# Performance work log

Hardware: AMD Instinct MI355X
Metric: run time of the kernel (lower is better)

Reference implementation:

```python
import jax, jax.numpy as jnp
import numpy as np
import math

B, S, DIM, H = 2, 2048, 1024, 16
DH = DIM // H          # 64, per-head dim
DFF = 2048             # FCLayer hidden
NEG = -1.0e9


def setup_inputs() -> dict:
    key = jax.random.key(0)
    ks = jax.random.split(key, 10)
    glorot = jax.nn.initializers.glorot_uniform()
    de_x = jax.random.normal(ks[0], (B, S, DIM), dtype=jnp.float32)
    en_x = jax.random.normal(ks[1], (B, S, DIM), dtype=jnp.float32)
    # causal mask: 1.0 where attention is disallowed (upper triangle)
    mask = jnp.triu(jnp.ones((S, S), dtype=jnp.float32), k=1)
    # Stacked per-head projection weights for the (shared) attn_heads.
    Wq = glorot(ks[2], (H, DIM, DH), jnp.float32)
    Wk = glorot(ks[3], (H, DIM, DH), jnp.float32)
    Wv = glorot(ks[4], (H, DIM, DH), jnp.float32)
    W1 = glorot(ks[5], (DIM, DFF), jnp.float32)
    b1 = jnp.zeros((DFF,), jnp.float32)
    W2 = glorot(ks[6], (DFF, DIM), jnp.float32)
    b2 = jnp.zeros((DIM,), jnp.float32)
    return {"de_x": de_x, "en_x": en_x, "mask": mask,
            "Wq": Wq, "Wk": Wk, "Wv": Wv,
            "W1": W1, "b1": b1, "W2": W2, "b2": b2}


def _multihead(q_x, k_x, v_x, Wq, Wk, Wv, mask):
    # q_x/k_x/v_x: [B,S,DIM]; W*: [H,DIM,DH]
    q = jnp.einsum('bsd,hde->bhse', q_x, Wq)
    k = jnp.einsum('bsd,hde->bhse', k_x, Wk)
    v = jnp.einsum('bsd,hde->bhse', v_x, Wv)
    p = jnp.einsum('bhse,bhte->bhst', q, k) / math.sqrt(DH)
    if mask is not None:
        p = p + mask * NEG
    p = jax.nn.softmax(p, axis=-1)
    h = jnp.einsum('bhst,bhte->bhse', p, v)      # [B,H,S,DH]
    # concat heads along feature dim -> [B,S,DIM]
    return h.transpose(0, 2, 1, 3).reshape(q_x.shape[0], q_x.shape[1], -1)


def reference(de_x, en_x, mask, Wq, Wk, Wv, W1, b1, W2, b2):
    # Faithful to the source: compute_multihead_output ignores its attn_heads
    # arg and always uses self.attn_heads, and binds head(q=outer_en, k=outer_en,
    # v=outer_de). So:
    #   h1 = MHA(q=de_x, k=de_x, v=de_x, mask) with attn_heads weights
    #   h2 = MHA(q=en_x, k=en_x, v=h1, None)   with the SAME weights
    h1 = _multihead(de_x, de_x, de_x, Wq, Wk, Wv, mask)
    h2 = _multihead(en_x, en_x, h1, Wq, Wk, Wv, None)
    ff1 = jax.nn.relu(h2 @ W1 + b1)
    y = ff1 @ W2 + b2
    return y
```

## Files before the change

### kernel.cpp

```cpp
#include <hip/hip_runtime.h>
#include <stdint.h>


#define DEV static __device__ __forceinline__

typedef __attribute__((ext_vector_type(8))) __bf16 bf16x8;
typedef __attribute__((ext_vector_type(8))) unsigned short u16x8;
typedef __attribute__((ext_vector_type(2))) uint32_t u32x2;
typedef __attribute__((ext_vector_type(4))) float f32x4;

DEV float bf2f(uint16_t u) { union { uint32_t u; float f; } v; v.u = ((uint32_t)u) << 16; return v.f; }
DEV uint16_t f2bf(float f) {
  union { float f; uint32_t u; } v; v.f = f;
  uint32_t r = v.u + 0x7fffu + ((v.u >> 16) & 1u);
  return (uint16_t)(r >> 16);
}
DEV uint16_t f2bf_hw(float f) { return __builtin_bit_cast(unsigned short, (__bf16)f); }

DEV bf16x8 asbf(u16x8 v) { return __builtin_bit_cast(bf16x8, v); }
DEV f32x4 mfma32(bf16x8 a, bf16x8 b, f32x4 c) {
  return __builtin_amdgcn_mfma_f32_16x16x32_bf16(a, b, c, 0, 0, 0);
}

DEV void gload_lds16(const void* g, void* l) {
  __builtin_amdgcn_global_load_lds(
      (const __attribute__((address_space(1))) uint32_t*)g,
      (__attribute__((address_space(3))) uint32_t*)l, 16, 0, 0);
}

DEV int swz(int row, int slot) { return slot ^ (row & 7); }

DEV bf16x8 frag8(const uint16_t* l, int row, int slot) {
  u16x8 v = *(const u16x8*)((const char*)l + row * 128 + (swz(row, slot) << 4));
  return asbf(v);
}

__global__ void probe_k(const uint32_t* __restrict__ mask, uint32_t* __restrict__ flag) {
  flag[0] = (mask[1] & 0xFFFFu) ? 1u : 0u;
}

__global__ __launch_bounds__(256) void cvt_k(const void* __restrict__ src,
                                             uint16_t* __restrict__ dst, int n,
                                             const uint32_t* __restrict__ flag) {
  const int isbf = (int)flag[0];
  const int stride = gridDim.x * 256 * 8;
  for (int i = (blockIdx.x * 256 + threadIdx.x) * 8; i < n; i += stride) {
    if (isbf) {
      *(u16x8*)(dst + i) = *(const u16x8*)((const uint16_t*)src + i);
    } else {
      const float* sf = (const float*)src + i;
      u16x8 o;
      for (int j = 0; j < 8; j++) o[j] = f2bf(sf[j]);
      *(u16x8*)(dst + i) = o;
    }
  }
}

__global__ __launch_bounds__(256) void transpose_k(const void* __restrict__ in_,
                                                   uint16_t* __restrict__ out, int R, int C,
                                                   float scale,
                                                   const uint32_t* __restrict__ flag) {
  __shared__ uint16_t t[32][33];
  const int isbf = (int)flag[0];
  const int b = blockIdx.z;
  const float* in_f = (const float*)in_ + (size_t)b * R * C;
  const uint16_t* in_u = (const uint16_t*)in_ + (size_t)b * R * C;
  out += (size_t)b * R * C;
  const int c0 = blockIdx.x * 32, r0 = blockIdx.y * 32;
  const int tx = threadIdx.x & 31, ty = threadIdx.x >> 5;
  for (int i = 0; i < 4; i++) {
    int r = ty + i * 8;
    size_t idx = (size_t)(r0 + r) * C + c0 + tx;
    uint16_t v;
    if (isbf) v = (scale == 1.0f) ? in_u[idx] : f2bf(bf2f(in_u[idx]) * scale);
    else      v = f2bf(in_f[idx] * scale);
    t[r][tx] = v;
  }
  __syncthreads();
  for (int i = 0; i < 4; i++) {
    int r = ty + i * 8;
    out[(size_t)(c0 + r) * R + r0 + tx] = t[tx][r];
  }
}

__global__ __launch_bounds__(256) void proj_k(
    const uint16_t* __restrict__ A_qk, const uint16_t* __restrict__ A_v,
    const uint16_t* __restrict__ Wt,
    uint16_t* __restrict__ Q, uint16_t* __restrict__ K, uint16_t* __restrict__ Vt) {
  __shared__ __attribute__((aligned(16))) uint16_t lA[2][128 * 64];
  __shared__ __attribute__((aligned(16))) uint16_t lB[2][128 * 64];
  const int tid = threadIdx.x, lane = tid & 63, wave = tid >> 6;
  const int g = lane >> 4;
  const int m0 = blockIdx.x * 128, n0 = blockIdx.y * 128;
  const int proj = n0 >> 10;
  const uint16_t* A = (proj == 2 ? A_v : A_qk);
  const uint16_t* Bt = Wt + (size_t)n0 * 1024;
  const int wm = wave >> 1, wn = wave & 1;
  f32x4 acc[4][4] = {};
  const int lrow = lane >> 3, sl = lane & 7;
  auto STAGE = [&](int buf, int kt) {
    for (int i = 0; i < 4; i++) {
      int cb = (i * 4 + wave) * 64;
      int row = (cb >> 3) + lrow;
      int so = swz(row, sl) << 3;
      gload_lds16(A + (size_t)(m0 + row) * 1024 + kt + so, &lA[buf][cb * 8]);
      gload_lds16(Bt + (size_t)row * 1024 + kt + so, &lB[buf][cb * 8]);
    }
  };
  STAGE(0, 0);
  int cur = 0;
  for (int it = 0; it < 16; it++) {
    __syncthreads();
    if (it + 1 < 16) STAGE(cur ^ 1, (it + 1) * 64);
    for (int kk = 0; kk < 2; kk++) {
      bf16x8 af[4], bfr[4];
      for (int fm = 0; fm < 4; fm++) af[fm] = frag8(lA[cur], wm * 64 + fm * 16 + (lane & 15), kk * 4 + g);
      for (int fn = 0; fn < 4; fn++) bfr[fn] = frag8(lB[cur], wn * 64 + fn * 16 + (lane & 15), kk * 4 + g);
      for (int fm = 0; fm < 4; fm++)
        for (int fn = 0; fn < 4; fn++)
          acc[fm][fn] = mfma32(af[fm], bfr[fn], acc[fm][fn]);
    }
    cur ^= 1;
  }
  if (proj != 2) {
    uint16_t* outp = (proj == 0 ? Q : K);
    for (int fm = 0; fm < 4; fm++)
      for (int fn = 0; fn < 4; fn++)
        for (int r = 0; r < 4; r++) {
          int row = m0 + wm * 64 + fm * 16 + g * 4 + r;
          int b = row >> 11, s = row & 2047;
          int col = n0 + wn * 64 + fn * 16 + (lane & 15);
          int h = (col >> 6) & 15, e = col & 63;
          outp[(((size_t)(b * 16 + h)) * 2048 + s) * 64 + e] = f2bf(acc[fm][fn][r]);
        }
  } else {
    __syncthreads();
    uint16_t* tv = &lA[0][0];
    for (int fm = 0; fm < 4; fm++)
      for (int fn = 0; fn < 4; fn++)
        for (int r = 0; r < 4; r++) {
          int rl = wm * 64 + fm * 16 + g * 4 + r;
          int cl = wn * 64 + fn * 16 + (lane & 15);
          int byte = rl * 2;
          *(uint16_t*)((char*)tv + cl * 256 + ((((byte >> 4)) ^ (cl & 15)) << 4) + (byte & 15)) =
              f2bf(acc[fm][fn][r]);
        }
    __syncthreads();
    const int b = m0 >> 11, s0 = m0 & 2047;
    const int c = tid >> 1, half = tid & 1;
    const int col = n0 + c;
    const int h = (col >> 6) & 15, e = col & 63;
    uint16_t* dst = Vt + (((size_t)(b * 16 + h)) * 64 + e) * 2048 + s0 + half * 64;
    for (int j = 0; j < 8; j++) {
      int rl = half * 64 + j * 8;
      u16x8 v = *(const u16x8*)((const char*)tv + c * 256 + (((rl >> 3) ^ (c & 15)) << 4));
      *(u16x8*)(dst + j * 8) = v;
    }
  }
}

template <int CAUSAL>
__global__ __launch_bounds__(256) void attn_k(const uint16_t* __restrict__ Q,
                                              const uint16_t* __restrict__ K,
                                              const uint16_t* __restrict__ Vt,
                                              uint16_t* __restrict__ Op0,
                                              uint16_t* __restrict__ Op1,
                                              float* __restrict__ lbuf) {
  __shared__ __attribute__((aligned(16))) uint16_t lK[2][64 * 64];
  __shared__ __attribute__((aligned(16))) uint16_t lV[2][64 * 64];
  __shared__ __attribute__((aligned(16))) uint16_t lP[4][16 * 64];
  const int tid = threadIdx.x, lane = tid & 63, wave = tid >> 6;
  const int g = lane >> 4;
  const int bx = blockIdx.x, h = blockIdx.y, b = blockIdx.z;
  int qt, split, kt0, kt1;
  if (CAUSAL) {
    if (bx < 32) {
      qt = 31 - (bx >> 1);
      split = bx & 1;
      int n0 = (qt + 1) >> 1;
      kt0 = split ? n0 : 0;
      kt1 = split ? (qt + 1) : n0;
    } else {
      qt = 47 - bx; split = 0; kt0 = 0; kt1 = qt + 1;
    }
  } else {
    qt = bx & 31; split = bx >> 5; kt0 = split * 16; kt1 = kt0 + 16;
  }
  const size_t bh = (size_t)(b * 16 + h);
  const uint16_t* Qg = Q + bh * 2048 * 64;
  const uint16_t* Kg = K + bh * 2048 * 64;
  const uint16_t* Vg = Vt + bh * 64 * 2048;
  uint16_t* lPw = lP[wave];
  bf16x8 ones;
  for (int j = 0; j < 8; j++) ones[j] = (__bf16)1.0f;
  const int lrow = lane >> 3, sl = lane & 7;
  auto STAGE = [&](int buf, int kt) {
    for (int i = 0; i < 2; i++) {
      int cb = (i * 4 + wave) * 64;
      int row = (cb >> 3) + lrow;
      int so = swz(row, sl) << 3;
      gload_lds16(Kg + (size_t)(kt * 64 + row) * 64 + so, &lK[buf][cb * 8]);
      gload_lds16(Vg + (size_t)row * 2048 + kt * 64 + so, &lV[buf][cb * 8]);
    }
  };
  const int q0 = qt * 64;
  bf16x8 qf[2];
  {
    int row = q0 + wave * 16 + (lane & 15);
    for (int kk = 0; kk < 2; kk++)
      qf[kk] = asbf(*(const u16x8*)(Qg + (size_t)row * 64 + kk * 32 + g * 8));
  }
  f32x4 oacc[4] = {};
  f32x4 acc_l = {};
  const int qrow = lane & 15;
  STAGE(0, kt0);
  int buf = 0;
  for (int kt = kt0; kt < kt1; kt++) {
    __syncthreads();
    if (kt + 1 < kt1) STAGE(buf ^ 1, kt + 1);
    f32x4 s[4] = {};
    for (int kk = 0; kk < 2; kk++)
      for (int nf = 0; nf < 4; nf++)
        s[nf] = mfma32(frag8(lK[buf], nf * 16 + (lane & 15), kk * 4 + g), qf[kk], s[nf]);
    if (CAUSAL && kt == qt) {
      for (int nf = 0; nf < 4; nf++)
        for (int r = 0; r < 4; r++) {
          int kloc = nf * 16 + g * 4 + r;
          if (kloc > wave * 16 + qrow) s[nf][r] = -1e9f;
        }
    }
    for (int nf = 0; nf < 4; nf++) {
      float p0 = __builtin_amdgcn_exp2f(s[nf][0]);
      float p1 = __builtin_amdgcn_exp2f(s[nf][1]);
      float p2 = __builtin_amdgcn_exp2f(s[nf][2]);
      float p3 = __builtin_amdgcn_exp2f(s[nf][3]);
      u32x2 w;
      w[0] = ((uint32_t)f2bf_hw(p1) << 16) | f2bf_hw(p0);
      w[1] = ((uint32_t)f2bf_hw(p3) << 16) | f2bf_hw(p2);
      int slot = 2 * nf + (g >> 1);
      *(u32x2*)((char*)lPw + qrow * 128 + ((slot ^ (qrow & 7)) << 4) + ((g & 1) << 3)) = w;
    }
    for (int kk = 0; kk < 2; kk++) {
      bf16x8 pa = frag8(lPw, qrow, kk * 4 + g);
      acc_l = mfma32(pa, ones, acc_l);
      for (int df = 0; df < 4; df++)
        oacc[df] = mfma32(pa, frag8(lV[buf], df * 16 + (lane & 15), kk * 4 + g), oacc[df]);
    }
    buf ^= 1;
  }
  uint16_t* Op = split ? Op1 : Op0;
  for (int df = 0; df < 4; df++)
    for (int r = 0; r < 4; r++) {
      int srow = q0 + wave * 16 + g * 4 + r;
      int e = df * 16 + (lane & 15);
      Op[((size_t)b * 2048 + srow) * 1024 + h * 64 + e] = f2bf(oacc[df][r]);
    }
  if ((lane & 15) == 0) {
    for (int r = 0; r < 4; r++) {
      int srow = q0 + wave * 16 + g * 4 + r;
      lbuf[((size_t)(split * 2 + b) * 16 + h) * 2048 + srow] = acc_l[r];
    }
  }
}

template <int CAUSAL>
__global__ __launch_bounds__(256) void merge_k(const uint16_t* __restrict__ O0,
                                               const uint16_t* __restrict__ O1,
                                               const float* __restrict__ lbuf,
                                               uint16_t* __restrict__ out) {
  int i = (blockIdx.x * 256 + threadIdx.x) * 8;
  int sg = i >> 10;
  int b = sg >> 11, s = sg & 2047;
  int h = (i & 1023) >> 6;
  size_t i0 = ((size_t)b * 16 + h) * 2048 + s;
  size_t i1 = ((size_t)(2 + b) * 16 + h) * 2048 + s;
  float l0 = lbuf[i0];
  u16x8 o0 = *(const u16x8*)(O0 + i);
  bool two = CAUSAL ? ((s >> 6) >= 16) : true;
  u16x8 o;
  if (two) {
    float inv = 1.f / (l0 + lbuf[i1]);
    u16x8 o1v = *(const u16x8*)(O1 + i);
    for (int j = 0; j < 8; j++)
      o[j] = f2bf((bf2f(o0[j]) + bf2f(o1v[j])) * inv);
  } else {
    float inv = 1.f / l0;
    for (int j = 0; j < 8; j++) o[j] = f2bf(bf2f(o0[j]) * inv);
  }
  *(u16x8*)(out + i) = o;
}

template <int RELU>
__global__ __launch_bounds__(256) void ff_k(const uint16_t* __restrict__ A,
                                            const uint16_t* __restrict__ Bt,
                                            const uint16_t* __restrict__ bias,
                                            uint16_t* __restrict__ C, int Kdim, int N) {
  __shared__ __attribute__((aligned(16))) uint16_t lA[2][128 * 64];
  __shared__ __attribute__((aligned(16))) uint16_t lB[2][128 * 64];
  const int tid = threadIdx.x, lane = tid & 63, wave = tid >> 6;
  const int g = lane >> 4;
  const int m0 = blockIdx.x * 128, n0 = blockIdx.y * 128;
  const int wm = wave >> 1, wn = wave & 1;
  f32x4 acc[4][4] = {};
  const int lrow = lane >> 3, sl = lane & 7;
  auto STAGE = [&](int buf, int kt) {
    for (int i = 0; i < 4; i++) {
      int cb = (i * 4 + wave) * 64;
      int row = (cb >> 3) + lrow;
      int so = swz(row, sl) << 3;
      gload_lds16(A + (size_t)(m0 + row) * Kdim + kt + so, &lA[buf][cb * 8]);
      gload_lds16(Bt + (size_t)(n0 + row) * Kdim + kt + so, &lB[buf][cb * 8]);
    }
  };
  STAGE(0, 0);
  int cur = 0;
  const int nit = Kdim >> 6;
  for (int it = 0; it < nit; it++) {
    __syncthreads();
    if (it + 1 < nit) STAGE(cur ^ 1, (it + 1) * 64);
    for (int kk = 0; kk < 2; kk++) {
      bf16x8 af[4], bfr[4];
      for (int fm = 0; fm < 4; fm++) af[fm] = frag8(lA[cur], wm * 64 + fm * 16 + (lane & 15), kk * 4 + g);
      for (int fn = 0; fn < 4; fn++) bfr[fn] = frag8(lB[cur], wn * 64 + fn * 16 + (lane & 15), kk * 4 + g);
      for (int fm = 0; fm < 4; fm++)
        for (int fn = 0; fn < 4; fn++)
          acc[fm][fn] = mfma32(af[fm], bfr[fn], acc[fm][fn]);
    }
    cur ^= 1;
  }
  for (int fm = 0; fm < 4; fm++)
    for (int fn = 0; fn < 4; fn++) {
      int col = n0 + wn * 64 + fn * 16 + (lane & 15);
      float bv = bf2f(bias[col]);
      for (int r = 0; r < 4; r++) {
        int row = m0 + wm * 64 + fm * 16 + g * 4 + r;
        float v = acc[fm][fn][r] + bv;
        if (RELU) v = fmaxf(v, 0.f);
        C[(size_t)row * N + col] = f2bf(v);
      }
    }
}

__global__ __launch_bounds__(256) void store_k(const uint16_t* __restrict__ yb,
                                               void* __restrict__ out, int n,
                                               const uint32_t* __restrict__ flag) {
  const int isbf = (int)flag[0];
  const int stride = gridDim.x * 256 * 8;
  for (int i = (blockIdx.x * 256 + threadIdx.x) * 8; i < n; i += stride) {
    u16x8 v = *(const u16x8*)(yb + i);
    if (isbf) {
      *(u16x8*)((uint16_t*)out + i) = v;
    } else {
      float* of = (float*)out + i;
      for (int j = 0; j < 8; j++) of[j] = bf2f(v[j]);
    }
  }
}

extern "C" void kernel_launch(void* const* d_in, const int* in_sizes, int n_in,
                              void* d_out, int out_size, void* d_ws, size_t ws_size,
                              hipStream_t stream) {
  const void* de_x = d_in[0];
  const void* en_x = d_in[1];
  const void* mask = d_in[2];
  const void* Wq = d_in[3];
  const void* Wk = d_in[4];
  const void* Wv = d_in[5];
  const void* W1 = d_in[6];
  const void* b1 = d_in[7];
  const void* W2 = d_in[8];
  const void* b2 = d_in[9];

  uint16_t* ws = (uint16_t*)d_ws;
  const size_t M1 = (size_t)1 << 20;
  uint32_t* flag = (uint32_t*)ws;
  uint16_t* b1c = ws + 1024;
  uint16_t* b2c = ws + 4096;
  float* lbuf = (float*)(ws + 8192);
  uint16_t* Wtq = ws + 1 * M1;
  uint16_t* Wtk = ws + 2 * M1;
  uint16_t* Wtv = ws + 3 * M1;
  uint16_t* W1t = ws + 4 * M1;
  uint16_t* W2t = ws + 6 * M1;
  uint16_t* de_c = ws + 8 * M1;
  uint16_t* en_c = ws + 12 * M1;
  uint16_t* Qb  = ws + 16 * M1;
  uint16_t* Kb  = ws + 20 * M1;
  uint16_t* Vtb = ws + 24 * M1;
  uint16_t* h1  = ws + 28 * M1;
  uint16_t* h2  = ws + 32 * M1;
  uint16_t* ff1 = Qb;
  uint16_t* yb  = Vtb;
  uint16_t* Op0 = de_c;
  uint16_t* Op1a = h2;
  uint16_t* Op1b = h1;

  const int NX = 2 * 2048 * 1024;
  dim3 blk(256);

  probe_k<<<1, 1, 0, stream>>>((const uint32_t*)mask, flag);
  cvt_k<<<2048, blk, 0, stream>>>(de_x, de_c, NX, flag);
  cvt_k<<<2048, blk, 0, stream>>>(en_x, en_c, NX, flag);
  cvt_k<<<1, blk, 0, stream>>>(b1, b1c, 2048, flag);
  cvt_k<<<1, blk, 0, stream>>>(b2, b2c, 1024, flag);
  transpose_k<<<dim3(2, 32, 16), blk, 0, stream>>>(Wq, Wtq, 1024, 64, 0.180336880f, flag);
  transpose_k<<<dim3(2, 32, 16), blk, 0, stream>>>(Wk, Wtk, 1024, 64, 1.0f, flag);
  transpose_k<<<dim3(2, 32, 16), blk, 0, stream>>>(Wv, Wtv, 1024, 64, 1.0f, flag);
  transpose_k<<<dim3(64, 32, 1), blk, 0, stream>>>(W1, W1t, 1024, 2048, 1.0f, flag);
  transpose_k<<<dim3(32, 64, 1), blk, 0, stream>>>(W2, W2t, 2048, 1024, 1.0f, flag);
  proj_k<<<dim3(32, 24), blk, 0, stream>>>(de_c, de_c, Wtq, Qb, Kb, Vtb);
  attn_k<1><<<dim3(48, 16, 2), blk, 0, stream>>>(Qb, Kb, Vtb, Op0, Op1a, lbuf);
  merge_k<1><<<2048, blk, 0, stream>>>(Op0, Op1a, lbuf, h1);
  proj_k<<<dim3(32, 24), blk, 0, stream>>>(en_c, h1, Wtq, Qb, Kb, Vtb);
  attn_k<0><<<dim3(64, 16, 2), blk, 0, stream>>>(Qb, Kb, Vtb, Op0, Op1b, lbuf);
  merge_k<0><<<2048, blk, 0, stream>>>(Op0, Op1b, lbuf, h2);
  ff_k<1><<<dim3(32, 16), blk, 0, stream>>>(h2, W1t, b1c, ff1, 1024, 2048);
  ff_k<0><<<dim3(32, 8), blk, 0, stream>>>(ff1, W2t, b2c, yb, 2048, 1024);
  store_k<<<2048, blk, 0, stream>>>(yb, d_out, out_size, flag);
}
```

Measured before the change: 294.3 us.

## Merge QKV weight transposes, drop bias converts, stage GEMM tiles through registers

```diff
diff --git a/kernel.cpp b/kernel.cpp
--- a/kernel.cpp
+++ b/kernel.cpp
@@ -42,17 +42,13 @@
 __global__ __launch_bounds__(256) void cvt_k(const void* __restrict__ src,
                                              uint16_t* __restrict__ dst, int n,
                                              const uint32_t* __restrict__ flag) {
-  const int isbf = (int)flag[0];
+  if (flag[0]) return;
   const int stride = gridDim.x * 256 * 8;
   for (int i = (blockIdx.x * 256 + threadIdx.x) * 8; i < n; i += stride) {
-    if (isbf) {
-      *(u16x8*)(dst + i) = *(const u16x8*)((const uint16_t*)src + i);
-    } else {
-      const float* sf = (const float*)src + i;
-      u16x8 o;
-      for (int j = 0; j < 8; j++) o[j] = f2bf(sf[j]);
-      *(u16x8*)(dst + i) = o;
-    }
+    const float* sf = (const float*)src + i;
+    u16x8 o;
+    for (int j = 0; j < 8; j++) o[j] = f2bf(sf[j]);
+    *(u16x8*)(dst + i) = o;
   }
 }
 
@@ -83,35 +79,79 @@
   }
 }
 
+__global__ __launch_bounds__(256) void transpose_qkv_k(const void* __restrict__ Wq,
+                                                       const void* __restrict__ Wk,
+                                                       const void* __restrict__ Wv,
+                                                       uint16_t* __restrict__ out,
+                                                       const uint32_t* __restrict__ flag) {
+  __shared__ uint16_t t[32][33];
+  const int isbf = (int)flag[0];
+  const int which = blockIdx.z >> 4, hh = blockIdx.z & 15;
+  const void* in_ = (which == 0 ? Wq : which == 1 ? Wk : Wv);
+  const float scale = (which == 0) ? 0.180336880f : 1.0f;
+  const int R = 1024, C = 64;
+  const float* in_f = (const float*)in_ + (size_t)hh * R * C;
+  const uint16_t* in_u = (const uint16_t*)in_ + (size_t)hh * R * C;
+  out += ((size_t)which * 16 + hh) * R * C;
+  const int c0 = blockIdx.x * 32, r0 = blockIdx.y * 32;
+  const int tx = threadIdx.x & 31, ty = threadIdx.x >> 5;
+  for (int i = 0; i < 4; i++) {
+    int r = ty + i * 8;
+    size_t idx = (size_t)(r0 + r) * C + c0 + tx;
+    uint16_t v;
+    if (isbf) v = (scale == 1.0f) ? in_u[idx] : f2bf(bf2f(in_u[idx]) * scale);
+    else      v = f2bf(in_f[idx] * scale);
+    t[r][tx] = v;
+  }
+  __syncthreads();
+  for (int i = 0; i < 4; i++) {
+    int r = ty + i * 8;
+    out[(size_t)(c0 + r) * R + r0 + tx] = t[tx][r];
+  }
+}
+
 __global__ __launch_bounds__(256) void proj_k(
-    const uint16_t* __restrict__ A_qk, const uint16_t* __restrict__ A_v,
+    const uint16_t* __restrict__ Aqk_c, const void* __restrict__ Aqk_r,
+    const uint16_t* __restrict__ Av_c, const void* __restrict__ Av_r,
     const uint16_t* __restrict__ Wt,
-    uint16_t* __restrict__ Q, uint16_t* __restrict__ K, uint16_t* __restrict__ Vt) {
+    uint16_t* __restrict__ Q, uint16_t* __restrict__ K, uint16_t* __restrict__ Vt,
+    const uint32_t* __restrict__ flag) {
   __shared__ __attribute__((aligned(16))) uint16_t lA[2][128 * 64];
   __shared__ __attribute__((aligned(16))) uint16_t lB[2][128 * 64];
+  const int isbf = (int)flag[0];
+  const uint16_t* Aqk = isbf ? (const uint16_t*)Aqk_r : Aqk_c;
+  const uint16_t* Av  = isbf ? (const uint16_t*)Av_r  : Av_c;
   const int tid = threadIdx.x, lane = tid & 63, wave = tid >> 6;
   const int g = lane >> 4;
   const int m0 = blockIdx.x * 128, n0 = blockIdx.y * 128;
   const int proj = n0 >> 10;
-  const uint16_t* A = (proj == 2 ? A_v : A_qk);
+  const uint16_t* A = (proj == 2 ? Av : Aqk);
   const uint16_t* Bt = Wt + (size_t)n0 * 1024;
   const int wm = wave >> 1, wn = wave & 1;
   f32x4 acc[4][4] = {};
-  const int lrow = lane >> 3, sl = lane & 7;
-  auto STAGE = [&](int buf, int kt) {
+  u16x8 ra[4], rb[4];
+  const int row0 = tid >> 3, slot0 = tid & 7;
+  auto loadT = [&](int kt) {
     for (int i = 0; i < 4; i++) {
-      int cb = (i * 4 + wave) * 64;
-      int row = (cb >> 3) + lrow;
-      int so = swz(row, sl) << 3;
-      gload_lds16(A + (size_t)(m0 + row) * 1024 + kt + so, &lA[buf][cb * 8]);
-      gload_lds16(Bt + (size_t)row * 1024 + kt + so, &lB[buf][cb * 8]);
+      int row = row0 + i * 32;
+      ra[i] = *(const u16x8*)(A + (size_t)(m0 + row) * 1024 + kt + slot0 * 8);
+      rb[i] = *(const u16x8*)(Bt + (size_t)row * 1024 + kt + slot0 * 8);
     }
   };
-  STAGE(0, 0);
+  auto writeT = [&](int buf) {
+    for (int i = 0; i < 4; i++) {
+      int row = row0 + i * 32;
+      *(u16x8*)&lA[buf][(row * 8 + swz(row, slot0)) * 8] = ra[i];
+      *(u16x8*)&lB[buf][(row * 8 + swz(row, slot0)) * 8] = rb[i];
+    }
+  };
+  loadT(0);
+  writeT(0);
   int cur = 0;
   for (int it = 0; it < 16; it++) {
+    const int more = (it < 15);
+    if (more) loadT((it + 1) * 64);
     __syncthreads();
-    if (it + 1 < 16) STAGE(cur ^ 1, (it + 1) * 64);
     for (int kk = 0; kk < 2; kk++) {
       bf16x8 af[4], bfr[4];
       for (int fm = 0; fm < 4; fm++) af[fm] = frag8(lA[cur], wm * 64 + fm * 16 + (lane & 15), kk * 4 + g);
@@ -120,6 +160,7 @@
         for (int fn = 0; fn < 4; fn++)
           acc[fm][fn] = mfma32(af[fm], bfr[fn], acc[fm][fn]);
     }
+    if (more) writeT(cur ^ 1);
     cur ^= 1;
   }
   if (proj != 2) {
@@ -135,7 +176,7 @@
         }
   } else {
     __syncthreads();
-    uint16_t* tv = &lA[0][0];
+    uint16_t* tv = (uint16_t*)lA;
     for (int fm = 0; fm < 4; fm++)
       for (int fn = 0; fn < 4; fn++)
         for (int r = 0; r < 4; r++) {
@@ -293,31 +334,41 @@
 template <int RELU>
 __global__ __launch_bounds__(256) void ff_k(const uint16_t* __restrict__ A,
                                             const uint16_t* __restrict__ Bt,
-                                            const uint16_t* __restrict__ bias,
-                                            uint16_t* __restrict__ C, int Kdim, int N) {
+                                            const void* __restrict__ bias,
+                                            uint16_t* __restrict__ C, int Kdim, int N,
+                                            const uint32_t* __restrict__ flag) {
   __shared__ __attribute__((aligned(16))) uint16_t lA[2][128 * 64];
   __shared__ __attribute__((aligned(16))) uint16_t lB[2][128 * 64];
+  const int isbf = (int)flag[0];
   const int tid = threadIdx.x, lane = tid & 63, wave = tid >> 6;
   const int g = lane >> 4;
   const int m0 = blockIdx.x * 128, n0 = blockIdx.y * 128;
   const int wm = wave >> 1, wn = wave & 1;
   f32x4 acc[4][4] = {};
-  const int lrow = lane >> 3, sl = lane & 7;
-  auto STAGE = [&](int buf, int kt) {
+  u16x8 ra[4], rb[4];
+  const int row0 = tid >> 3, slot0 = tid & 7;
+  auto loadT = [&](int kt) {
     for (int i = 0; i < 4; i++) {
-      int cb = (i * 4 + wave) * 64;
-      int row = (cb >> 3) + lrow;
-      int so = swz(row, sl) << 3;
-      gload_lds16(A + (size_t)(m0 + row) * Kdim + kt + so, &lA[buf][cb * 8]);
-      gload_lds16(Bt + (size_t)(n0 + row) * Kdim + kt + so, &lB[buf][cb * 8]);
+      int row = row0 + i * 32;
+      ra[i] = *(const u16x8*)(A + (size_t)(m0 + row) * Kdim + kt + slot0 * 8);
+      rb[i] = *(const u16x8*)(Bt + (size_t)(n0 + row) * Kdim + kt + slot0 * 8);
     }
   };
-  STAGE(0, 0);
+  auto writeT = [&](int buf) {
+    for (int i = 0; i < 4; i++) {
+      int row = row0 + i * 32;
+      *(u16x8*)&lA[buf][(row * 8 + swz(row, slot0)) * 8] = ra[i];
+      *(u16x8*)&lB[buf][(row * 8 + swz(row, slot0)) * 8] = rb[i];
+    }
+  };
+  loadT(0);
+  writeT(0);
   int cur = 0;
   const int nit = Kdim >> 6;
   for (int it = 0; it < nit; it++) {
+    const int more = (it < nit - 1);
+    if (more) loadT((it + 1) * 64);
     __syncthreads();
-    if (it + 1 < nit) STAGE(cur ^ 1, (it + 1) * 64);
     for (int kk = 0; kk < 2; kk++) {
       bf16x8 af[4], bfr[4];
       for (int fm = 0; fm < 4; fm++) af[fm] = frag8(lA[cur], wm * 64 + fm * 16 + (lane & 15), kk * 4 + g);
@@ -326,12 +377,13 @@
         for (int fn = 0; fn < 4; fn++)
           acc[fm][fn] = mfma32(af[fm], bfr[fn], acc[fm][fn]);
     }
+    if (more) writeT(cur ^ 1);
     cur ^= 1;
   }
   for (int fm = 0; fm < 4; fm++)
     for (int fn = 0; fn < 4; fn++) {
       int col = n0 + wn * 64 + fn * 16 + (lane & 15);
-      float bv = bf2f(bias[col]);
+      float bv = isbf ? bf2f(((const uint16_t*)bias)[col]) : ((const float*)bias)[col];
       for (int r = 0; r < 4; r++) {
         int row = m0 + wm * 64 + fm * 16 + g * 4 + r;
         float v = acc[fm][fn][r] + bv;
@@ -374,12 +426,8 @@
   uint16_t* ws = (uint16_t*)d_ws;
   const size_t M1 = (size_t)1 << 20;
   uint32_t* flag = (uint32_t*)ws;
-  uint16_t* b1c = ws + 1024;
-  uint16_t* b2c = ws + 4096;
   float* lbuf = (float*)(ws + 8192);
   uint16_t* Wtq = ws + 1 * M1;
-  uint16_t* Wtk = ws + 2 * M1;
-  uint16_t* Wtv = ws + 3 * M1;
   uint16_t* W1t = ws + 4 * M1;
   uint16_t* W2t = ws + 6 * M1;
   uint16_t* de_c = ws + 8 * M1;
@@ -401,20 +449,16 @@
   probe_k<<<1, 1, 0, stream>>>((const uint32_t*)mask, flag);
   cvt_k<<<2048, blk, 0, stream>>>(de_x, de_c, NX, flag);
   cvt_k<<<2048, blk, 0, stream>>>(en_x, en_c, NX, flag);
-  cvt_k<<<1, blk, 0, stream>>>(b1, b1c, 2048, flag);
-  cvt_k<<<1, blk, 0, stream>>>(b2, b2c, 1024, flag);
-  transpose_k<<<dim3(2, 32, 16), blk, 0, stream>>>(Wq, Wtq, 1024, 64, 0.180336880f, flag);
-  transpose_k<<<dim3(2, 32, 16), blk, 0, stream>>>(Wk, Wtk, 1024, 64, 1.0f, flag);
-  transpose_k<<<dim3(2, 32, 16), blk, 0, stream>>>(Wv, Wtv, 1024, 64, 1.0f, flag);
+  transpose_qkv_k<<<dim3(2, 32, 48), blk, 0, stream>>>(Wq, Wk, Wv, Wtq, flag);
   transpose_k<<<dim3(64, 32, 1), blk, 0, stream>>>(W1, W1t, 1024, 2048, 1.0f, flag);
   transpose_k<<<dim3(32, 64, 1), blk, 0, stream>>>(W2, W2t, 2048, 1024, 1.0f, flag);
-  proj_k<<<dim3(32, 24), blk, 0, stream>>>(de_c, de_c, Wtq, Qb, Kb, Vtb);
+  proj_k<<<dim3(32, 24), blk, 0, stream>>>(de_c, de_x, de_c, de_x, Wtq, Qb, Kb, Vtb, flag);
   attn_k<1><<<dim3(48, 16, 2), blk, 0, stream>>>(Qb, Kb, Vtb, Op0, Op1a, lbuf);
   merge_k<1><<<2048, blk, 0, stream>>>(Op0, Op1a, lbuf, h1);
-  proj_k<<<dim3(32, 24), blk, 0, stream>>>(en_c, h1, Wtq, Qb, Kb, Vtb);
+  proj_k<<<dim3(32, 24), blk, 0, stream>>>(en_c, en_x, h1, h1, Wtq, Qb, Kb, Vtb, flag);
   attn_k<0><<<dim3(64, 16, 2), blk, 0, stream>>>(Qb, Kb, Vtb, Op0, Op1b, lbuf);
   merge_k<0><<<2048, blk, 0, stream>>>(Op0, Op1b, lbuf, h2);
-  ff_k<1><<<dim3(32, 16), blk, 0, stream>>>(h2, W1t, b1c, ff1, 1024, 2048);
-  ff_k<0><<<dim3(32, 8), blk, 0, stream>>>(ff1, W2t, b2c, yb, 2048, 1024);
+  ff_k<1><<<dim3(32, 16), blk, 0, stream>>>(h2, W1t, b1, ff1, 1024, 2048, flag);
+  ff_k<0><<<dim3(32, 8), blk, 0, stream>>>(ff1, W2t, b2, yb, 2048, 1024, flag);
   store_k<<<2048, blk, 0, stream>>>(yb, d_out, out_size, flag);
 }
```

Result: faster. 271.4 us (-7.8%).
